# Kernel tuning notes

Measured on AMD Instinct MI355X. Metric: run time of the kernel, lower is better.

The kernel has to match this reference:

```python
import jax, jax.numpy as jnp
import numpy as np

B, S, D, H = 16, 4800, 256, 8
Dh = D // H
ATTN_EPS = 1e-6   # LinearAttention eps
LN_EPS = 1e-5     # nn.LayerNorm default eps


def _layer_norm(x, g, b):
    m = jnp.mean(x, axis=-1, keepdims=True)
    v = jnp.mean((x - m) ** 2, axis=-1, keepdims=True)
    return (x - m) * jax.lax.rsqrt(v + LN_EPS) * g + b


def setup_inputs() -> dict:
    key = jax.random.key(0)
    ks = jax.random.split(key, 8)
    sc_d = 1.0 / np.sqrt(D)
    sc_2d = 1.0 / np.sqrt(2 * D)
    return {
        "x": jax.random.normal(ks[0], (B, S, D), jnp.float32),
        "source": jax.random.normal(ks[1], (B, S, D), jnp.float32),
        "x_mask": jnp.ones((B, S), bool),
        "source_mask": jnp.ones((B, S), bool),
        # torch nn.Linear weights are [out_features, in_features]
        "Wq": jax.random.normal(ks[2], (D, D), jnp.float32) * sc_d,
        "Wk": jax.random.normal(ks[3], (D, D), jnp.float32) * sc_d,
        "Wv": jax.random.normal(ks[4], (D, D), jnp.float32) * sc_d,
        "Wm": jax.random.normal(ks[5], (D, D), jnp.float32) * sc_d,
        "W1": jax.random.normal(ks[6], (2 * D, 2 * D), jnp.float32) * sc_2d,
        "W2": jax.random.normal(ks[7], (D, 2 * D), jnp.float32) * sc_2d,
        "g_attn": jnp.ones((D,), jnp.float32),
        "b_attn": jnp.zeros((D,), jnp.float32),
        "g_ffn": jnp.ones((D,), jnp.float32),
        "b_ffn": jnp.zeros((D,), jnp.float32),
    }


def reference(x, source, x_mask, source_mask, Wq, Wk, Wv, Wm, W1, W2,
              g_attn, b_attn, g_ffn, b_ffn):
    Bn, Sn, Dm = x.shape
    # QKV projections (bias-free), split into heads: [B, S, H, Dh]
    q = (x @ Wq.T).reshape(Bn, Sn, H, Dh)
    k = (source @ Wk.T).reshape(Bn, Sn, H, Dh)
    v = (source @ Wv.T).reshape(Bn, Sn, H, Dh)
    # elu feature map
    q = jax.nn.elu(q) + 1.0
    k = jax.nn.elu(k) + 1.0
    qm = x_mask[:, :, None, None].astype(q.dtype)
    km = source_mask[:, :, None, None].astype(k.dtype)
    q = q * qm
    k = k * km
    v = v * km
    v = v / Sn
    # linear attention: kv outer product [B, H, Dh, Dh]
    kv = jnp.einsum('nshd,nshv->nhdv', k, v)
    z = 1.0 / (jnp.einsum('nlhd,nhd->nlh', q, k.sum(axis=1)) + ATTN_EPS)
    msg = jnp.einsum('nlhd,nhdv,nlh->nlhv', q, kv, z) * Sn  # [B, S, H, Dh]
    # merge + norm
    msg = msg.reshape(Bn, Sn, Dm) @ Wm.T
    msg = _layer_norm(msg, g_attn, b_attn)
    # FFN on concat([x, message]) -> 2D -> relu -> D, then norm
    h = jnp.concatenate([x, msg], axis=-1)
    h = jax.nn.relu(h @ W1.T) @ W2.T
    h = _layer_norm(h, g_ffn, b_ffn)
    return x + h
```

## Files before the change

### kernel.cpp

```cpp
#include <hip/hip_runtime.h>
#include <math.h>

#define BB 16
#define SS 4800
#define DD 256
#define HH 8
#define M_ROWS (BB * SS)
#define ATTN_EPS 1e-6f
#define LN_EPS 1e-5f
#define NCHUNK 10

typedef __attribute__((ext_vector_type(8))) __bf16 bf16x8;
typedef __attribute__((ext_vector_type(4))) float floatx4;
typedef unsigned short ushort;
typedef unsigned int uint;

__device__ __forceinline__ ushort f2bf(float f) {
    uint u = __builtin_bit_cast(uint, f);
    return (ushort)((u + 0x7fffu + ((u >> 16) & 1u)) >> 16);
}
__device__ __forceinline__ float bf2f(ushort h) {
    return __builtin_bit_cast(float, (uint)h << 16);
}
__device__ __forceinline__ void gload16(const ushort* g, ushort* l) {
    __builtin_amdgcn_global_load_lds(
        (const __attribute__((address_space(1))) uint*)g,
        (__attribute__((address_space(3))) uint*)l, 16, 0, 0);
}

__global__ __launch_bounds__(256) void mgemm(
    const ushort* __restrict__ A, int lda,
    const ushort* __restrict__ W, int ldw,
    float* __restrict__ Cf, ushort* __restrict__ Ch, int ldc,
    int K, int epi)
{
    __shared__ ushort As[128 * 32];
    __shared__ ushort Bs[128 * 32];
    const int tid = threadIdx.x;
    const int lane = tid & 63, wave = tid >> 6;
    const int wm = (wave & 1) * 64, wn = (wave >> 1) * 64;
    const int bm = blockIdx.x * 128, bn = blockIdx.y * 128;

    floatx4 acc[4][4] = {};

    const int srow_base = 32 * wave;
    const int lrow = lane >> 2;
    const int koff = (lane & 3) * 8;

    for (int k0 = 0; k0 < K; k0 += 32) {
#pragma unroll
        for (int c = 0; c < 2; ++c) {
            int row = srow_base + 16 * c + lrow;
            gload16(A + (size_t)(bm + row) * lda + k0 + koff, &As[(srow_base + 16 * c) * 32]);
            gload16(W + (size_t)(bn + row) * ldw + k0 + koff, &Bs[(srow_base + 16 * c) * 32]);
        }
        __syncthreads();
        const int fr = lane & 15, fk = (lane >> 4) * 8;
        bf16x8 a[4], b[4];
#pragma unroll
        for (int i = 0; i < 4; ++i) a[i] = *(const bf16x8*)&As[(wm + i * 16 + fr) * 32 + fk];
#pragma unroll
        for (int j = 0; j < 4; ++j) b[j] = *(const bf16x8*)&Bs[(wn + j * 16 + fr) * 32 + fk];
#pragma unroll
        for (int i = 0; i < 4; ++i)
#pragma unroll
            for (int j = 0; j < 4; ++j)
                acc[i][j] = __builtin_amdgcn_mfma_f32_16x16x32_bf16(a[i], b[j], acc[i][j], 0, 0, 0);
        __syncthreads();
    }

    const int cr = (lane >> 4) * 4, cc = lane & 15;
#pragma unroll
    for (int i = 0; i < 4; ++i)
#pragma unroll
        for (int j = 0; j < 4; ++j) {
            int m = bm + wm + i * 16 + cr;
            int n = bn + wn + j * 16 + cc;
#pragma unroll
            for (int r = 0; r < 4; ++r) {
                float v = acc[i][j][r];
                if (epi == 1)      v = (v > 0.f) ? (v + 1.f) : __expf(v);
                else if (epi == 2) v = (v > 0.f) ? v : 0.f;
                if (Ch) Ch[(size_t)(m + r) * ldc + n] = f2bf(v);
                else    Cf[(size_t)(m + r) * ldc + n] = v;
            }
        }
}

__global__ __launch_bounds__(256) void attn_kernel(
    const ushort* __restrict__ q,
    const float* __restrict__ KV,
    const float* __restrict__ KS,
    ushort* __restrict__ msg)
{
    __shared__ float kvs[8 * 1028];
    __shared__ float kss[32 * 8];
    const int tid = threadIdx.x;
    const int bm = blockIdx.x * 64;
    const int b = bm / SS;

    for (int i = tid; i < 8192; i += 256) {
        int h = i >> 10, de = i & 1023;
        kvs[h * 1028 + de] = KV[(size_t)b * 8192 + i];
    }
    if (tid < 256) {
        int h = tid >> 5, d = tid & 31;
        kss[d * 8 + h] = KS[b * 256 + h * 32 + d];
    }
    __syncthreads();

    const int h = tid & 7;
    const int r0 = tid >> 3;
    const size_t m0 = bm + r0, m1 = bm + r0 + 32;

    float acc0[32] = {};
    float acc1[32] = {};
    float z0 = 0.f, z1 = 0.f;

    const uint4* q0p = (const uint4*)(q + m0 * 256 + h * 32);
    const uint4* q1p = (const uint4*)(q + m1 * 256 + h * 32);
    const float* kvh = &kvs[h * 1028];
    const float* ksh = &kss[h];

#pragma unroll
    for (int db = 0; db < 4; ++db) {
        uint4 qw0 = q0p[db];
        uint4 qw1 = q1p[db];
        uint qu0[4] = {qw0.x, qw0.y, qw0.z, qw0.w};
        uint qu1[4] = {qw1.x, qw1.y, qw1.z, qw1.w};
#pragma unroll
        for (int dd = 0; dd < 8; ++dd) {
            int d = db * 8 + dd;
            float qd0 = bf2f((ushort)(qu0[dd >> 1] >> ((dd & 1) * 16)));
            float qd1 = bf2f((ushort)(qu1[dd >> 1] >> ((dd & 1) * 16)));
            z0 += qd0 * ksh[d * 8];
            z1 += qd1 * ksh[d * 8];
            const float* kvd = kvh + d * 32;
#pragma unroll
            for (int e4 = 0; e4 < 8; ++e4) {
                float4 kv = *(const float4*)(kvd + e4 * 4);
                acc0[e4 * 4 + 0] += qd0 * kv.x; acc1[e4 * 4 + 0] += qd1 * kv.x;
                acc0[e4 * 4 + 1] += qd0 * kv.y; acc1[e4 * 4 + 1] += qd1 * kv.y;
                acc0[e4 * 4 + 2] += qd0 * kv.z; acc1[e4 * 4 + 2] += qd1 * kv.z;
                acc0[e4 * 4 + 3] += qd0 * kv.w; acc1[e4 * 4 + 3] += qd1 * kv.w;
            }
        }
    }

    float zi0 = 1.f / (z0 + ATTN_EPS);
    float zi1 = 1.f / (z1 + ATTN_EPS);
    uint4* o0 = (uint4*)(msg + m0 * 256 + h * 32);
    uint4* o1 = (uint4*)(msg + m1 * 256 + h * 32);
#pragma unroll
    for (int c = 0; c < 4; ++c) {
        uint4 pk;
        pk.x = (uint)f2bf(acc0[c*8+0]*zi0) | ((uint)f2bf(acc0[c*8+1]*zi0) << 16);
        pk.y = (uint)f2bf(acc0[c*8+2]*zi0) | ((uint)f2bf(acc0[c*8+3]*zi0) << 16);
        pk.z = (uint)f2bf(acc0[c*8+4]*zi0) | ((uint)f2bf(acc0[c*8+5]*zi0) << 16);
        pk.w = (uint)f2bf(acc0[c*8+6]*zi0) | ((uint)f2bf(acc0[c*8+7]*zi0) << 16);
        o0[c] = pk;
        pk.x = (uint)f2bf(acc1[c*8+0]*zi1) | ((uint)f2bf(acc1[c*8+1]*zi1) << 16);
        pk.y = (uint)f2bf(acc1[c*8+2]*zi1) | ((uint)f2bf(acc1[c*8+3]*zi1) << 16);
        pk.z = (uint)f2bf(acc1[c*8+4]*zi1) | ((uint)f2bf(acc1[c*8+5]*zi1) << 16);
        pk.w = (uint)f2bf(acc1[c*8+6]*zi1) | ((uint)f2bf(acc1[c*8+7]*zi1) << 16);
        o1[c] = pk;
    }
}

__global__ __launch_bounds__(256) void kv_part_kernel(
    const ushort* __restrict__ k, const ushort* __restrict__ v,
    float* __restrict__ kvp, float* __restrict__ ksp)
{
    __shared__ float ks[16][32];
    __shared__ float vs[16][32];
    const int bh = blockIdx.x;
    const int chunk = blockIdx.y;
    const int b = bh >> 3, h = bh & 7;
    const int tid = threadIdx.x;
    const int d = tid >> 3;
    const int e0 = (tid & 7) * 4;
    const int s_base = chunk * (SS / NCHUNK);
    float acc[4] = {0.f, 0.f, 0.f, 0.f};
    float ksacc = 0.f;
    const int sl = tid >> 4;
    const int dd = (tid & 15) * 2;

    for (int s0 = 0; s0 < SS / NCHUNK; s0 += 16) {
        size_t off = ((size_t)(b * SS + s_base + s0 + sl)) * 256 + h * 32 + dd;
        uint ku = *(const uint*)(k + off);
        uint vu = *(const uint*)(v + off);
        ks[sl][dd] = bf2f((ushort)ku); ks[sl][dd + 1] = bf2f((ushort)(ku >> 16));
        vs[sl][dd] = bf2f((ushort)vu); vs[sl][dd + 1] = bf2f((ushort)(vu >> 16));
        __syncthreads();
#pragma unroll
        for (int s = 0; s < 16; ++s) {
            float kd = ks[s][d];
            ksacc += kd;
#pragma unroll
            for (int j = 0; j < 4; ++j) acc[j] += kd * vs[s][e0 + j];
        }
        __syncthreads();
    }
    size_t base = ((size_t)bh * NCHUNK + chunk) * 1024;
#pragma unroll
    for (int j = 0; j < 4; ++j) kvp[base + d * 32 + e0 + j] = acc[j];
    if ((tid & 7) == 0) ksp[((size_t)bh * NCHUNK + chunk) * 32 + d] = ksacc;
}

__global__ __launch_bounds__(256) void kv_reduce_kernel(
    const float* __restrict__ kvp, const float* __restrict__ ksp,
    float* __restrict__ kv, float* __restrict__ ksum)
{
    const int bh = blockIdx.x;
    const int tid = threadIdx.x;
    for (int idx = tid; idx < 1024; idx += 256) {
        float s = 0.f;
        for (int c = 0; c < NCHUNK; ++c)
            s += kvp[((size_t)bh * NCHUNK + c) * 1024 + idx];
        kv[(size_t)bh * 1024 + idx] = s;
    }
    if (tid < 32) {
        float s = 0.f;
        for (int c = 0; c < NCHUNK; ++c)
            s += ksp[((size_t)bh * NCHUNK + c) * 32 + tid];
        ksum[bh * 32 + tid] = s;
    }
}

__global__ __launch_bounds__(256) void ln_kernel(
    const float* __restrict__ in, const float* __restrict__ res,
    const float* __restrict__ g, const float* __restrict__ bt,
    float* __restrict__ outf, ushort* __restrict__ outh, int old, int ooff,
    int nrows)
{
    const int lane = threadIdx.x & 63;
    const int nwaves = (gridDim.x * blockDim.x) >> 6;
    const float4 gv = ((const float4*)g)[lane];
    const float4 bv = ((const float4*)bt)[lane];
    for (int row = (blockIdx.x * blockDim.x + threadIdx.x) >> 6; row < nrows;
         row += nwaves) {
        float4 v = ((const float4*)(in + (size_t)row * 256))[lane];
        float s = (v.x + v.y) + (v.z + v.w);
#pragma unroll
        for (int o = 1; o < 64; o <<= 1) s += __shfl_xor(s, o);
        float mean = s * (1.f / 256);
        float dx = v.x - mean, dy = v.y - mean, dz = v.z - mean, dw = v.w - mean;
        float q = (dx * dx + dy * dy) + (dz * dz + dw * dw);
#pragma unroll
        for (int o = 1; o < 64; o <<= 1) q += __shfl_xor(q, o);
        float rs = rsqrtf(q * (1.f / 256) + LN_EPS);
        float rx = dx * rs * gv.x + bv.x;
        float ry = dy * rs * gv.y + bv.y;
        float rz = dz * rs * gv.z + bv.z;
        float rw = dw * rs * gv.w + bv.w;
        if (res) {
            float4 rr = ((const float4*)(res + (size_t)row * 256))[lane];
            rx += rr.x; ry += rr.y; rz += rr.z; rw += rr.w;
        }
        if (outh) {
            uint2 pk;
            pk.x = (uint)f2bf(rx) | ((uint)f2bf(ry) << 16);
            pk.y = (uint)f2bf(rz) | ((uint)f2bf(rw) << 16);
            *(uint2*)(outh + (size_t)row * old + ooff + lane * 4) = pk;
        } else {
            float4 o4 = {rx, ry, rz, rw};
            *(float4*)(outf + (size_t)row * old + ooff + lane * 4) = o4;
        }
    }
}

__global__ __launch_bounds__(256) void cvt_flat(const float* __restrict__ src,
                                                ushort* __restrict__ dst, int n4)
{
    int i = blockIdx.x * 256 + threadIdx.x;
    if (i >= n4) return;
    float4 f = ((const float4*)src)[i];
    uint2 pk;
    pk.x = (uint)f2bf(f.x) | ((uint)f2bf(f.y) << 16);
    pk.y = (uint)f2bf(f.z) | ((uint)f2bf(f.w) << 16);
    ((uint2*)dst)[i] = pk;
}

__global__ __launch_bounds__(256) void cvt_x(const float* __restrict__ src,
                                             ushort* __restrict__ dst)
{
    int i = blockIdx.x * 256 + threadIdx.x;
    int row = i >> 6, c4 = i & 63;
    float4 f = ((const float4*)src)[i];
    uint2 pk;
    pk.x = (uint)f2bf(f.x) | ((uint)f2bf(f.y) << 16);
    pk.y = (uint)f2bf(f.z) | ((uint)f2bf(f.w) << 16);
    *(uint2*)(dst + (size_t)row * 512 + c4 * 4) = pk;
}

extern "C" void kernel_launch(void* const* d_in, const int* in_sizes, int n_in,
                              void* d_out, int out_size, void* d_ws, size_t ws_size,
                              hipStream_t stream)
{
    const float* x      = (const float*)d_in[0];
    const float* source = (const float*)d_in[1];
    const float* Wq = (const float*)d_in[4];
    const float* Wk = (const float*)d_in[5];
    const float* Wv = (const float*)d_in[6];
    const float* Wm = (const float*)d_in[7];
    const float* W1 = (const float*)d_in[8];
    const float* W2 = (const float*)d_in[9];
    const float* g_attn = (const float*)d_in[10];
    const float* b_attn = (const float*)d_in[11];
    const float* g_ffn  = (const float*)d_in[12];
    const float* b_ffn  = (const float*)d_in[13];
    float* out = (float*)d_out;

    char* p = (char*)d_ws;
    ushort* XC  = (ushort*)p;                 p += (size_t)M_ROWS * 512 * 2;
    ushort* SK  = (ushort*)p;                 p += (size_t)M_ROWS * 256 * 2;
    ushort* KVA = (ushort*)p;                 p += (size_t)M_ROWS * 512 * 2;
    float*  Tf  = (float*)p;                  p += (size_t)M_ROWS * 256 * 4;
    float*  PKV = (float*)p;                  p += (size_t)BB * HH * NCHUNK * 1024 * 4;
    float*  PKS = (float*)p;                  p += (size_t)BB * HH * NCHUNK * 32 * 4;
    float*  KV  = (float*)p;                  p += (size_t)BB * HH * 1024 * 4;
    float*  KS  = (float*)p;                  p += (size_t)BB * HH * 32 * 4;
    ushort* WB  = (ushort*)p;
    ushort* Wqb = WB;
    ushort* Wkb = WB + 65536;
    ushort* Wvb = WB + 131072;
    ushort* Wmb = WB + 196608;
    ushort* W1b = WB + 262144;
    ushort* W2b = WB + 524288;
    ushort* Kb  = KVA;
    ushort* Vb  = KVA + (size_t)M_ROWS * 256;
    ushort* Hid = KVA;

    dim3 blk(256);

    cvt_x   <<<M_ROWS * 64 / 256, blk, 0, stream>>>(x, XC);
    cvt_flat<<<M_ROWS * 64 / 256, blk, 0, stream>>>(source, SK, M_ROWS * 64);
    cvt_flat<<<64,  blk, 0, stream>>>(Wq, Wqb, 16384);
    cvt_flat<<<64,  blk, 0, stream>>>(Wk, Wkb, 16384);
    cvt_flat<<<64,  blk, 0, stream>>>(Wv, Wvb, 16384);
    cvt_flat<<<64,  blk, 0, stream>>>(Wm, Wmb, 16384);
    cvt_flat<<<256, blk, 0, stream>>>(W1, W1b, 65536);
    cvt_flat<<<128, blk, 0, stream>>>(W2, W2b, 32768);

    mgemm<<<dim3(600, 2), blk, 0, stream>>>(SK, 256, Wkb, 256, nullptr, Kb, 256, 256, 1);
    mgemm<<<dim3(600, 2), blk, 0, stream>>>(SK, 256, Wvb, 256, nullptr, Vb, 256, 256, 0);

    kv_part_kernel<<<dim3(BB * HH, NCHUNK), blk, 0, stream>>>(Kb, Vb, PKV, PKS);
    kv_reduce_kernel<<<BB * HH, blk, 0, stream>>>(PKV, PKS, KV, KS);

    mgemm<<<dim3(600, 2), blk, 0, stream>>>(XC, 512, Wqb, 256, nullptr, SK, 256, 256, 1);

    attn_kernel<<<M_ROWS / 64, blk, 0, stream>>>(SK, KV, KS, Kb);

    mgemm<<<dim3(600, 2), blk, 0, stream>>>(Kb, 256, Wmb, 256, Tf, nullptr, 256, 256, 0);
    ln_kernel<<<2048, blk, 0, stream>>>(Tf, nullptr, g_attn, b_attn, nullptr, XC, 512, 256, M_ROWS);

    mgemm<<<dim3(600, 4), blk, 0, stream>>>(XC, 512, W1b, 512, nullptr, Hid, 512, 512, 2);
    mgemm<<<dim3(600, 2), blk, 0, stream>>>(Hid, 512, W2b, 512, Tf, nullptr, 256, 512, 0);

    ln_kernel<<<2048, blk, 0, stream>>>(Tf, x, g_ffn, b_ffn, out, nullptr, 256, 0, M_ROWS);
}
```

Before: 622.4 us.

## Fuse K/V projections into one GEMM, bf16 intermediates, swap grid order

The K and V projections now run as a single GEMM with N=512, relying on Wk and Wv being contiguous in the weight buffer, and the epilogue applies elu+1 only to the first 256 columns. The kv partial kernel reads the interleaved KV buffer, and attention writes its output in place over Q. The Wm and W2 GEMM outputs are stored as bf16 instead of fp32 before LayerNorm, halving that traffic at some precision cost. The grid is transposed so blocks sharing an A row-tile run consecutively, which is meant to improve L2 reuse of A.

```diff
diff --git a/kernel.cpp b/kernel.cpp
--- a/kernel.cpp
+++ b/kernel.cpp
@@ -39,7 +39,7 @@
     const int tid = threadIdx.x;
     const int lane = tid & 63, wave = tid >> 6;
     const int wm = (wave & 1) * 64, wn = (wave >> 1) * 64;
-    const int bm = blockIdx.x * 128, bn = blockIdx.y * 128;
+    const int bm = blockIdx.y * 128, bn = blockIdx.x * 128;
 
     floatx4 acc[4][4] = {};
 
@@ -81,6 +81,7 @@
                 float v = acc[i][j][r];
                 if (epi == 1)      v = (v > 0.f) ? (v + 1.f) : __expf(v);
                 else if (epi == 2) v = (v > 0.f) ? v : 0.f;
+                else if (epi == 3) { if (n < 256) v = (v > 0.f) ? (v + 1.f) : __expf(v); }
                 if (Ch) Ch[(size_t)(m + r) * ldc + n] = f2bf(v);
                 else    Cf[(size_t)(m + r) * ldc + n] = v;
             }
@@ -88,10 +89,10 @@
 }
 
 __global__ __launch_bounds__(256) void attn_kernel(
-    const ushort* __restrict__ q,
+    const ushort* q,
     const float* __restrict__ KV,
     const float* __restrict__ KS,
-    ushort* __restrict__ msg)
+    ushort* msg)
 {
     __shared__ float kvs[8 * 1028];
     __shared__ float kss[32 * 8];
@@ -168,7 +169,7 @@
 }
 
 __global__ __launch_bounds__(256) void kv_part_kernel(
-    const ushort* __restrict__ k, const ushort* __restrict__ v,
+    const ushort* __restrict__ kvin,
     float* __restrict__ kvp, float* __restrict__ ksp)
 {
     __shared__ float ks[16][32];
@@ -186,9 +187,9 @@
     const int dd = (tid & 15) * 2;
 
     for (int s0 = 0; s0 < SS / NCHUNK; s0 += 16) {
-        size_t off = ((size_t)(b * SS + s_base + s0 + sl)) * 256 + h * 32 + dd;
-        uint ku = *(const uint*)(k + off);
-        uint vu = *(const uint*)(v + off);
+        size_t off = ((size_t)(b * SS + s_base + s0 + sl)) * 512 + h * 32 + dd;
+        uint ku = *(const uint*)(kvin + off);
+        uint vu = *(const uint*)(kvin + off + 256);
         ks[sl][dd] = bf2f((ushort)ku); ks[sl][dd + 1] = bf2f((ushort)(ku >> 16));
         vs[sl][dd] = bf2f((ushort)vu); vs[sl][dd + 1] = bf2f((ushort)(vu >> 16));
         __syncthreads();
@@ -228,7 +229,8 @@
 }
 
 __global__ __launch_bounds__(256) void ln_kernel(
-    const float* __restrict__ in, const float* __restrict__ res,
+    const float* __restrict__ in, const ushort* __restrict__ inh,
+    const float* __restrict__ res,
     const float* __restrict__ g, const float* __restrict__ bt,
     float* __restrict__ outf, ushort* __restrict__ outh, int old, int ooff,
     int nrows)
@@ -239,12 +241,20 @@
     const float4 bv = ((const float4*)bt)[lane];
     for (int row = (blockIdx.x * blockDim.x + threadIdx.x) >> 6; row < nrows;
          row += nwaves) {
-        float4 v = ((const float4*)(in + (size_t)row * 256))[lane];
-        float s = (v.x + v.y) + (v.z + v.w);
+        float vx, vy, vz, vw;
+        if (inh) {
+            uint2 u = *(const uint2*)(inh + (size_t)row * 256 + lane * 4);
+            vx = bf2f((ushort)u.x); vy = bf2f((ushort)(u.x >> 16));
+            vz = bf2f((ushort)u.y); vw = bf2f((ushort)(u.y >> 16));
+        } else {
+            float4 v = ((const float4*)(in + (size_t)row * 256))[lane];
+            vx = v.x; vy = v.y; vz = v.z; vw = v.w;
+        }
+        float s = (vx + vy) + (vz + vw);
 #pragma unroll
         for (int o = 1; o < 64; o <<= 1) s += __shfl_xor(s, o);
         float mean = s * (1.f / 256);
-        float dx = v.x - mean, dy = v.y - mean, dz = v.z - mean, dw = v.w - mean;
+        float dx = vx - mean, dy = vy - mean, dz = vz - mean, dw = vw - mean;
         float q = (dx * dx + dy * dy) + (dz * dz + dw * dw);
 #pragma unroll
         for (int o = 1; o < 64; o <<= 1) q += __shfl_xor(q, o);
@@ -327,9 +337,10 @@
     ushort* Wmb = WB + 196608;
     ushort* W1b = WB + 262144;
     ushort* W2b = WB + 524288;
-    ushort* Kb  = KVA;
-    ushort* Vb  = KVA + (size_t)M_ROWS * 256;
+    ushort* KVb = KVA;
+    ushort* Mrg = KVA;
     ushort* Hid = KVA;
+    ushort* Tb  = (ushort*)Tf;
 
     dim3 blk(256);
 
@@ -342,21 +353,22 @@
     cvt_flat<<<256, blk, 0, stream>>>(W1, W1b, 65536);
     cvt_flat<<<128, blk, 0, stream>>>(W2, W2b, 32768);
 
-    mgemm<<<dim3(600, 2), blk, 0, stream>>>(SK, 256, Wkb, 256, nullptr, Kb, 256, 256, 1);
-    mgemm<<<dim3(600, 2), blk, 0, stream>>>(SK, 256, Wvb, 256, nullptr, Vb, 256, 256, 0);
-
-    kv_part_kernel<<<dim3(BB * HH, NCHUNK), blk, 0, stream>>>(Kb, Vb, PKV, PKS);
+    mgemm<<<dim3(4, 600), blk, 0, stream>>>(SK, 256, Wkb, 256, nullptr, KVb, 512, 256, 3);
+
+    kv_part_kernel<<<dim3(BB * HH, NCHUNK), blk, 0, stream>>>(KVb, PKV, PKS);
     kv_reduce_kernel<<<BB * HH, blk, 0, stream>>>(PKV, PKS, KV, KS);
 
-    mgemm<<<dim3(600, 2), blk, 0, stream>>>(XC, 512, Wqb, 256, nullptr, SK, 256, 256, 1);
-
-    attn_kernel<<<M_ROWS / 64, blk, 0, stream>>>(SK, KV, KS, Kb);
-
-    mgemm<<<dim3(600, 2), blk, 0, stream>>>(Kb, 256, Wmb, 256, Tf, nullptr, 256, 256, 0);
-    ln_kernel<<<2048, blk, 0, stream>>>(Tf, nullptr, g_attn, b_attn, nullptr, XC, 512, 256, M_ROWS);
-
-    mgemm<<<dim3(600, 4), blk, 0, stream>>>(XC, 512, W1b, 512, nullptr, Hid, 512, 512, 2);
-    mgemm<<<dim3(600, 2), blk, 0, stream>>>(Hid, 512, W2b, 512, Tf, nullptr, 256, 512, 0);
-
-    ln_kernel<<<2048, blk, 0, stream>>>(Tf, x, g_ffn, b_ffn, out, nullptr, 256, 0, M_ROWS);
-}
+    mgemm<<<dim3(2, 600), blk, 0, stream>>>(XC, 512, Wqb, 256, nullptr, SK, 256, 256, 1);
+
+    attn_kernel<<<M_ROWS / 64, blk, 0, stream>>>(SK, KV, KS, SK);
+
+    mgemm<<<dim3(2, 600), blk, 0, stream>>>(SK, 256, Wmb, 256, nullptr, Mrg, 256, 256, 0);
+    ln_kernel<<<2048, blk, 0, stream>>>(nullptr, Mrg, nullptr, g_attn, b_attn,
+                                        nullptr, XC, 512, 256, M_ROWS);
+
+    mgemm<<<dim3(4, 600), blk, 0, stream>>>(XC, 512, W1b, 512, nullptr, Hid, 512, 512, 2);
+    mgemm<<<dim3(2, 600), blk, 0, stream>>>(Hid, 512, W2b, 512, nullptr, Tb, 256, 512, 0);
+
+    ln_kernel<<<2048, blk, 0, stream>>>(nullptr, Tb, x, g_ffn, b_ffn,
+                                        out, nullptr, 256, 0, M_ROWS);
+}
```

Result: no change. 629.4 us (+1.1%).
